# Kernel tuning notes

Measured on AMD Instinct MI355X. Metric: run time of the kernel, lower is better.

## Reference

```python
import jax, jax.numpy as jnp
import numpy as np

TAU = 1.0      # temperature for gumbel-softmax
EPS = 1e-12    # F.normalize eps


def _l2norm(v, axis):
    n = jnp.sqrt(jnp.sum(v * v, axis=axis, keepdims=True))
    return v / jnp.maximum(n, EPS)


def setup_inputs() -> dict:
    key = jax.random.key(0)
    k1, k2, k3, k4 = jax.random.split(key, 4)
    b, c, h, w, n = 8, 512, 64, 64, 1024
    x = jax.random.normal(k1, (b, c, h, w), dtype=jnp.float32)
    centers = jax.random.normal(k2, (n, c), dtype=jnp.float32)          # VQ codebook
    clusters = jax.random.normal(k3, (n, c), dtype=jnp.float32)         # ClusterLookup param
    gumbel_noise = jax.random.gumbel(k4, (b, n, h, w), dtype=jnp.float32)
    return {"x": x, "centers": centers, "clusters": clusters, "gumbel_noise": gumbel_noise}


def reference(x, centers, clusters, gumbel_noise):
    # similarity logits: [b, n, h, w]
    inner = jnp.einsum('bchw,nc->bnhw', x, centers)
    # hard gumbel-softmax (straight-through) over code dim
    y_soft = jax.nn.softmax((inner + gumbel_noise) / TAU, axis=1)
    idx = jnp.argmax(y_soft, axis=1)                                     # [b, h, w]
    y_hard = jax.nn.one_hot(idx, centers.shape[0], axis=1, dtype=y_soft.dtype)
    one_hot = y_hard - jax.lax.stop_gradient(y_soft) + y_soft            # [b, n, h, w]
    # quantized features: codebook lookup expressed as einsum
    z_q = jnp.einsum('bnhw,nd->bdhw', one_hot, centers)                  # [b, c, h, w]
    # ClusterLookup(z_q, alpha=None, is_direct=False)
    nf = _l2norm(z_q, axis=1)
    ncl = _l2norm(clusters, axis=1)
    ip = jnp.einsum('bchw,nc->bnhw', nf, ncl)                            # cluster logits
    preds = jnp.argmax(ip, axis=1)                                       # [b, h, w] int
    probs = jax.nn.one_hot(preds, clusters.shape[0], axis=1, dtype=ip.dtype)
    cluster_loss = -jnp.mean(jnp.sum(probs * ip, axis=1))
    return (cluster_loss, preds, ip, z_q)
```

## Files before the change

kernel.cpp:

```cpp
#include <hip/hip_runtime.h>
#include <math.h>

#define C 512
#define HW 4096
#define N 1024
#define NPIX 32768
#define MARGIN 2.0f
#define BLKPX 64
#define WAVES 4

typedef short s16x8 __attribute__((ext_vector_type(8)));
typedef float f32x4 __attribute__((ext_vector_type(4)));

__device__ inline unsigned short f2bf(float f) {
    unsigned int u = __float_as_uint(f);
    return (unsigned short)((u + 0x7FFFu + ((u >> 16) & 1u)) >> 16);
}
__device__ inline float h2f(unsigned short u) {
    _Float16 h; __builtin_memcpy(&h, &u, 2); return (float)h;
}
__device__ inline unsigned short f2h(float f) {
    _Float16 h = (_Float16)f; unsigned short u; __builtin_memcpy(&u, &h, 2); return u;
}
__device__ inline unsigned int mono(float v) {
    unsigned int u = __float_as_uint(v);
    return (u & 0x80000000u) ? ~u : (u | 0x80000000u);
}
__device__ inline int xsw(int p, int G) {
    return p * 512 + ((G ^ (((p >> 2) & 7) ^ ((p & 3) << 1))) << 2);
}

__global__ __launch_bounds__(64) void k_norms(const float* __restrict__ centers,
                                              const float* __restrict__ clusters,
                                              float* __restrict__ cnorm,
                                              float* __restrict__ clnorm) {
    int r = blockIdx.x;
    const float* src = (r < N) ? (centers + (size_t)r * C) : (clusters + (size_t)(r - N) * C);
    int lane = threadIdx.x;
    float s = 0.f;
    for (int k = lane; k < C; k += 64) { float v = src[k]; s += v * v; }
    #pragma unroll
    for (int m = 1; m < 64; m <<= 1) s += __shfl_xor(s, m, 64);
    if (lane == 0) {
        float nrm = sqrtf(s);
        if (nrm < 1e-12f) nrm = 1e-12f;
        if (r < N) cnorm[r] = nrm; else clnorm[r - N] = nrm;
    }
}

__global__ __launch_bounds__(256) void k_gemmM(const float* __restrict__ centers,
                                               const float* __restrict__ clusters,
                                               const float* __restrict__ cnorm,
                                               const float* __restrict__ clnorm,
                                               float* __restrict__ M) {
    __shared__ float as[32][68];
    __shared__ float bs[32][68];
    int tid = threadIdx.x;
    int tx = tid & 15, ty = tid >> 4;
    int i0 = blockIdx.x * 64, j0 = blockIdx.y * 64;
    int lrow = tid >> 2, lkq = (tid & 3) * 8;
    float acc[4][4] = {};
    for (int kc = 0; kc < C; kc += 32) {
        float4 a0 = *(const float4*)(centers + (size_t)(i0 + lrow) * C + kc + lkq);
        float4 a1 = *(const float4*)(centers + (size_t)(i0 + lrow) * C + kc + lkq + 4);
        float4 b0 = *(const float4*)(clusters + (size_t)(j0 + lrow) * C + kc + lkq);
        float4 b1 = *(const float4*)(clusters + (size_t)(j0 + lrow) * C + kc + lkq + 4);
        __syncthreads();
        as[lkq+0][lrow]=a0.x; as[lkq+1][lrow]=a0.y; as[lkq+2][lrow]=a0.z; as[lkq+3][lrow]=a0.w;
        as[lkq+4][lrow]=a1.x; as[lkq+5][lrow]=a1.y; as[lkq+6][lrow]=a1.z; as[lkq+7][lrow]=a1.w;
        bs[lkq+0][lrow]=b0.x; bs[lkq+1][lrow]=b0.y; bs[lkq+2][lrow]=b0.z; bs[lkq+3][lrow]=b0.w;
        bs[lkq+4][lrow]=b1.x; bs[lkq+5][lrow]=b1.y; bs[lkq+6][lrow]=b1.z; bs[lkq+7][lrow]=b1.w;
        __syncthreads();
        #pragma unroll
        for (int k = 0; k < 32; k += 4) {
            float av[4][4], bv[4][4];
            #pragma unroll
            for (int kk = 0; kk < 4; ++kk) {
                float4 ta = *(const float4*)&as[k+kk][tx*4];
                float4 tb = *(const float4*)&bs[k+kk][ty*4];
                av[kk][0]=ta.x; av[kk][1]=ta.y; av[kk][2]=ta.z; av[kk][3]=ta.w;
                bv[kk][0]=tb.x; bv[kk][1]=tb.y; bv[kk][2]=tb.z; bv[kk][3]=tb.w;
            }
            #pragma unroll
            for (int kk = 0; kk < 4; ++kk)
                #pragma unroll
                for (int ii = 0; ii < 4; ++ii)
                    #pragma unroll
                    for (int jj = 0; jj < 4; ++jj)
                        acc[ii][jj] = fmaf(av[kk][ii], bv[kk][jj], acc[ii][jj]);
        }
    }
    float rci[4], rcj[4];
    #pragma unroll
    for (int ii = 0; ii < 4; ++ii) rci[ii] = cnorm[i0 + tx*4 + ii];
    #pragma unroll
    for (int jj = 0; jj < 4; ++jj) rcj[jj] = clnorm[j0 + ty*4 + jj];
    #pragma unroll
    for (int ii = 0; ii < 4; ++ii)
        #pragma unroll
        for (int jj = 0; jj < 4; ++jj)
            M[(size_t)(i0 + tx*4 + ii) * N + (j0 + ty*4 + jj)] = acc[ii][jj] / (rci[ii] * rcj[jj]);
}

__global__ __launch_bounds__(256) void k_rowstat(const float* __restrict__ M,
                                                 float* __restrict__ rowmax,
                                                 int* __restrict__ rowarg) {
    __shared__ float sv[256];
    __shared__ int   sa[256];
    int i = blockIdx.x, tid = threadIdx.x;
    float bv = -INFINITY; int ba = 0;
    for (int j = tid; j < N; j += 256) {
        float v = M[(size_t)i * N + j];
        if (v > bv || (v == bv && j < ba)) { bv = v; ba = j; }
    }
    sv[tid] = bv; sa[tid] = ba;
    __syncthreads();
    for (int s = 128; s > 0; s >>= 1) {
        if (tid < s) {
            float v = sv[tid + s]; int a = sa[tid + s];
            if (v > sv[tid] || (v == sv[tid] && a < sa[tid])) { sv[tid] = v; sa[tid] = a; }
        }
        __syncthreads();
    }
    if (tid == 0) { rowmax[i] = sv[0]; rowarg[i] = sa[0]; }
}

__global__ __launch_bounds__(64) void k_cenfrag(const float* __restrict__ centers,
                                                unsigned short* __restrict__ cenB) {
    int f = blockIdx.x;
    int nt = f >> 4, kt = f & 15;
    int lane = threadIdx.x;
    int r = lane & 15, g = lane >> 4;
    const float* src = centers + (size_t)(nt * 16 + r) * C + kt * 32 + g * 4;
    float4 lo = *(const float4*)src;
    float4 hi = *(const float4*)(src + 16);
    union { unsigned short us[8]; uint4 q; } u;
    u.us[0]=f2bf(lo.x); u.us[1]=f2bf(lo.y); u.us[2]=f2bf(lo.z); u.us[3]=f2bf(lo.w);
    u.us[4]=f2bf(hi.x); u.us[5]=f2bf(hi.y); u.us[6]=f2bf(hi.z); u.us[7]=f2bf(hi.w);
    *(uint4*)(cenB + ((size_t)f * 64 + lane) * 8) = u.q;
}

__global__ __launch_bounds__(256, 1) void k_fused(const float* __restrict__ x,
                                                  const unsigned short* __restrict__ cenB,
                                                  const float* __restrict__ gumbel,
                                                  const float* __restrict__ centers,
                                                  int* __restrict__ idxb) {
    __shared__ float xs[BLKPX * 512];
    __shared__ unsigned short cen[16 * 512];
    __shared__ unsigned long long pixkey[BLKPX];
    __shared__ unsigned int candlist[WAVES][256];
    __shared__ int candcount[WAVES];

    int tid = threadIdx.x;
    int lane = tid & 63, w = tid >> 6;
    int r = lane & 15, g = lane >> 4;

    int p0 = blockIdx.x * BLKPX;
    int b = p0 >> 12, hw0 = p0 & (HW - 1);

    if (tid < BLKPX) pixkey[tid] = 0ull;
    if (tid < WAVES) candcount[tid] = 0;

    const uint4* cb = (const uint4*)cenB;
    uint4* cl = (uint4*)cen;
    #pragma unroll
    for (int j = 0; j < 4; ++j) cl[j * 256 + tid] = cb[j * 256 + tid];

    const float* xb = x + (size_t)b * C * HW + hw0;
    {
        int q = tid & 15, k0 = tid >> 4;
        #pragma unroll
        for (int kk = 0; kk < 32; ++kk) {
            int k = kk * 16 + k0;
            float4 v = *(const float4*)(xb + (size_t)k * HW + q * 4);
            int G = k >> 2, e = k & 3;
            xs[xsw(q * 4 + 0, G) + e] = v.x;
            xs[xsw(q * 4 + 1, G) + e] = v.y;
            xs[xsw(q * 4 + 2, G) + e] = v.z;
            xs[xsw(q * 4 + 3, G) + e] = v.w;
        }
    }
    __syncthreads();

    uint4 cr0 = cb[1024 + tid], cr1 = cb[1280 + tid], cr2 = cb[1536 + tid], cr3 = cb[1792 + tid];
    const float* gbase = gumbel + (size_t)b * N * HW + hw0 + w * 16 + g * 4;
    float4 gv_c = *(const float4*)(gbase + (size_t)r * HW);
    float4 gv_n = *(const float4*)(gbase + (size_t)(16 + r) * HW);

    s16x8 a[16];
    #pragma unroll
    for (int kt = 0; kt < 16; ++kt) {
        float4 lo = *(const float4*)&xs[xsw(w * 16 + r, kt * 8 + g)];
        float4 hi = *(const float4*)&xs[xsw(w * 16 + r, kt * 8 + 4 + g)];
        s16x8 t;
        t[0] = (short)f2bf(lo.x); t[1] = (short)f2bf(lo.y);
        t[2] = (short)f2bf(lo.z); t[3] = (short)f2bf(lo.w);
        t[4] = (short)f2bf(hi.x); t[5] = (short)f2bf(hi.y);
        t[6] = (short)f2bf(hi.z); t[7] = (short)f2bf(hi.w);
        a[kt] = t;
    }

    float m4[4] = {-INFINITY, -INFINITY, -INFINITY, -INFINITY};
    for (int ntc = 0; ntc < 8; ++ntc) {
        unsigned int keepH[16];
        #pragma unroll
        for (int s = 0; s < 8; ++s) {
            int nt = ntc * 8 + s;
            int ntf = (nt + 2 <= 63) ? nt + 2 : 63;
            float4 gv_f = *(const float4*)(gbase + (size_t)(ntf * 16 + r) * HW);
            const s16x8* bp = (const s16x8*)cen + lane;
            f32x4 acc0 = {0.f, 0.f, 0.f, 0.f};
            f32x4 acc1 = {0.f, 0.f, 0.f, 0.f};
            #pragma unroll
            for (int kt = 0; kt < 16; kt += 2) {
                s16x8 b0 = bp[kt * 64];
                s16x8 b1 = bp[(kt + 1) * 64];
                acc0 = __builtin_amdgcn_mfma_f32_16x16x32_bf16(a[kt],     b0, acc0, 0, 0, 0);
                acc1 = __builtin_amdgcn_mfma_f32_16x16x32_bf16(a[kt + 1], b1, acc1, 0, 0, 0);
            }
            float v0 = acc0[0] + acc1[0] + gv_c.x;
            float v1 = acc0[1] + acc1[1] + gv_c.y;
            float v2 = acc0[2] + acc1[2] + gv_c.z;
            float v3 = acc0[3] + acc1[3] + gv_c.w;
            m4[0] = fmaxf(m4[0], v0); m4[1] = fmaxf(m4[1], v1);
            m4[2] = fmaxf(m4[2], v2); m4[3] = fmaxf(m4[3], v3);
            keepH[s * 2]     = (unsigned int)f2h(v0) | ((unsigned int)f2h(v1) << 16);
            keepH[s * 2 + 1] = (unsigned int)f2h(v2) | ((unsigned int)f2h(v3) << 16);
            __builtin_amdgcn_s_barrier();
            __builtin_amdgcn_sched_barrier(0);
            cl[tid] = cr0; cl[256 + tid] = cr1; cl[512 + tid] = cr2; cl[768 + tid] = cr3;
            {
                const uint4* src = cb + (size_t)ntf * 1024;
                cr0 = src[tid]; cr1 = src[256 + tid]; cr2 = src[512 + tid]; cr3 = src[768 + tid];
            }
            asm volatile("s_waitcnt lgkmcnt(0)" ::: "memory");
            __builtin_amdgcn_s_barrier();
            __builtin_amdgcn_sched_barrier(0);
            gv_c = gv_n; gv_n = gv_f;
        }
        #pragma unroll
        for (int s2 = 1; s2 < 16; s2 <<= 1) {
            #pragma unroll
            for (int j = 0; j < 4; ++j) m4[j] = fmaxf(m4[j], __shfl_xor(m4[j], s2, 64));
        }
        float thr[4];
        #pragma unroll
        for (int j = 0; j < 4; ++j) thr[j] = m4[j] - MARGIN;
        #pragma unroll
        for (int s = 0; s < 8; ++s) {
            int nn = (ntc * 8 + s) * 16 + r;
            #pragma unroll
            for (int j2 = 0; j2 < 2; ++j2) {
                unsigned int pk = keepH[s * 2 + j2];
                float lo = h2f((unsigned short)(pk & 0xFFFFu));
                float hi = h2f((unsigned short)(pk >> 16));
                if (lo >= thr[j2 * 2]) {
                    int pos = atomicAdd(&candcount[w], 1);
                    if (pos < 256) candlist[w][pos] =
                        (unsigned int)nn | ((unsigned int)(w * 16 + g * 4 + j2 * 2) << 10);
                }
                if (hi >= thr[j2 * 2 + 1]) {
                    int pos = atomicAdd(&candcount[w], 1);
                    if (pos < 256) candlist[w][pos] =
                        (unsigned int)nn | ((unsigned int)(w * 16 + g * 4 + j2 * 2 + 1) << 10);
                }
            }
        }
    }

    int cc = candcount[w]; if (cc > 256) cc = 256;
    int sl = lane & 15, cg = lane >> 4;
    for (int t0 = 0; t0 < cc; t0 += 4) {
        int c = t0 + cg;
        bool valid = c < cc;
        unsigned int e = candlist[w][valid ? c : 0];
        int n = (int)(e & 1023u), pl = (int)(e >> 10);
        const float* cenr = centers + (size_t)n * C;
        float s = 0.f;
        #pragma unroll
        for (int m = 0; m < 8; ++m) {
            int G = sl + (m << 4);
            float4 xv = *(const float4*)&xs[xsw(pl, G)];
            float4 cv = *(const float4*)(cenr + (G << 2));
            s = fmaf(xv.x, cv.x, s); s = fmaf(xv.y, cv.y, s);
            s = fmaf(xv.z, cv.z, s); s = fmaf(xv.w, cv.w, s);
        }
        #pragma unroll
        for (int s2 = 1; s2 < 16; s2 <<= 1) s += __shfl_xor(s, s2, 64);
        if (valid && sl == 0) {
            float val = s + gumbel[((size_t)b * N + n) * HW + hw0 + pl];
            unsigned long long key = ((unsigned long long)mono(val) << 32) | (unsigned int)(1023 - n);
            atomicMax(&pixkey[pl], key);
        }
    }
    __syncthreads();
    if (tid < BLKPX) idxb[p0 + tid] = 1023 - (int)(unsigned int)(pixkey[tid] & 0xFFFFFFFFull);
}

__global__ __launch_bounds__(256) void k_preds(const int* __restrict__ idxb,
                                               const float* __restrict__ rowmax,
                                               const int* __restrict__ rowarg,
                                               float* __restrict__ preds_out,
                                               float* __restrict__ partial) {
    __shared__ float sv[256];
    int gid = blockIdx.x * 256 + threadIdx.x;
    int i = idxb[gid];
    preds_out[gid] = (float)rowarg[i];
    sv[threadIdx.x] = rowmax[i];
    __syncthreads();
    for (int s = 128; s > 0; s >>= 1) {
        if (threadIdx.x < s) sv[threadIdx.x] += sv[threadIdx.x + s];
        __syncthreads();
    }
    if (threadIdx.x == 0) partial[blockIdx.x] = sv[0];
}

__global__ __launch_bounds__(256) void k_gather(const float* __restrict__ src, int ncols,
                                                const int* __restrict__ idx,
                                                float* __restrict__ dst) {
    __shared__ float rows[64][65];
    int tile = blockIdx.x;
    int col0 = blockIdx.y * 64;
    int tid = threadIdx.x;
    int lane = tid & 63, w = tid >> 6;
    int b = tile >> 6, hw0 = (tile & 63) << 6;
    #pragma unroll
    for (int r8 = 0; r8 < 16; ++r8) {
        int r = w * 16 + r8;
        int row = idx[tile * 64 + r];
        rows[r][lane] = src[(size_t)row * ncols + col0 + lane];
    }
    __syncthreads();
    #pragma unroll
    for (int jj = 0; jj < 16; ++jj) {
        int j = col0 + w * 16 + jj;
        dst[((size_t)b * ncols + j) * HW + hw0 + lane] = rows[lane][w * 16 + jj];
    }
}

__global__ __launch_bounds__(128) void k_loss(const float* __restrict__ partial,
                                              float* __restrict__ out) {
    __shared__ float sv[128];
    sv[threadIdx.x] = partial[threadIdx.x];
    __syncthreads();
    for (int s = 64; s > 0; s >>= 1) {
        if (threadIdx.x < s) sv[threadIdx.x] += sv[threadIdx.x + s];
        __syncthreads();
    }
    if (threadIdx.x == 0) out[0] = -(sv[0] / 32768.0f);
}

extern "C" void kernel_launch(void* const* d_in, const int* in_sizes, int n_in,
                              void* d_out, int out_size, void* d_ws, size_t ws_size,
                              hipStream_t stream) {
    const float* x        = (const float*)d_in[0];
    const float* centers  = (const float*)d_in[1];
    const float* clusters = (const float*)d_in[2];
    const float* gumbel   = (const float*)d_in[3];
    float* out = (float*)d_out;

    char* w = (char*)d_ws;
    int*   idxb    = (int*)w;
    float* cnorm   = (float*)(w + 131072);
    float* clnorm  = cnorm + 1024;
    float* rowmax  = clnorm + 1024;
    int*   rowarg  = (int*)(rowmax + 1024);
    float* partial = (float*)(rowarg + 1024);
    float* M       = (float*)(w + 262144);
    unsigned short* cenB = (unsigned short*)(w + 4456448);

    float* out_loss  = out;
    float* out_preds = out + 1;
    float* out_ip    = out + 1 + 32768;
    float* out_zq    = out + 1 + 32768 + (size_t)N * NPIX;

    k_norms  <<<2048, 64, 0, stream>>>(centers, clusters, cnorm, clnorm);
    k_gemmM  <<<dim3(16, 16), 256, 0, stream>>>(centers, clusters, cnorm, clnorm, M);
    k_rowstat<<<1024, 256, 0, stream>>>(M, rowmax, rowarg);
    k_cenfrag<<<1024, 64, 0, stream>>>(centers, cenB);
    k_fused  <<<512, 256, 0, stream>>>(x, cenB, gumbel, centers, idxb);
    k_preds  <<<128, 256, 0, stream>>>(idxb, rowmax, rowarg, out_preds, partial);
    k_gather <<<dim3(512, 16), 256, 0, stream>>>(M, N, idxb, out_ip);
    k_gather <<<dim3(512, 8),  256, 0, stream>>>(centers, C, idxb, out_zq);
    k_loss   <<<1, 128, 0, stream>>>(partial, out_loss);
}
```

Baseline: 247.3 us.

## Pre-transpose x into pixel-major scratch and split codebook across wave groups

Adds a transpose kernel that writes x as pixel-major [pixel][channel] into the z_q output buffer, used as scratch. The fused argmax kernel then loads A fragments straight from global memory and drops the 128KB x tile from shared memory. It now runs 512 threads per block, with two wave groups each scanning half of the codebook, and double-buffers codebook fragments with one barrier per step. The aim is much higher occupancy and less LDS pressure, at the cost of an extra full pass over x to build the transpose and more syncthreads.

```diff
diff --git a/kernel.cpp b/kernel.cpp
--- a/kernel.cpp
+++ b/kernel.cpp
@@ -6,8 +6,6 @@
 #define N 1024
 #define NPIX 32768
 #define MARGIN 2.0f
-#define BLKPX 64
-#define WAVES 4
 
 typedef short s16x8 __attribute__((ext_vector_type(8)));
 typedef float f32x4 __attribute__((ext_vector_type(4)));
@@ -25,9 +23,6 @@
 __device__ inline unsigned int mono(float v) {
     unsigned int u = __float_as_uint(v);
     return (u & 0x80000000u) ? ~u : (u | 0x80000000u);
-}
-__device__ inline int xsw(int p, int G) {
-    return p * 512 + ((G ^ (((p >> 2) & 7) ^ ((p & 3) << 1))) << 2);
 }
 
 __global__ __launch_bounds__(64) void k_norms(const float* __restrict__ centers,
@@ -125,6 +120,29 @@
     if (tid == 0) { rowmax[i] = sv[0]; rowarg[i] = sa[0]; }
 }
 
+__global__ __launch_bounds__(256) void k_prepT(const float* __restrict__ x,
+                                               float* __restrict__ xT) {
+    __shared__ float t[64][65];
+    int bidx = blockIdx.x;
+    int pt = bidx & 63, kt = (bidx >> 6) & 7, b = bidx >> 9;
+    int r = threadIdx.x >> 4, c4 = (threadIdx.x & 15) * 4;
+    const float* src = x + ((size_t)b * C + kt * 64) * HW + pt * 64;
+    #pragma unroll
+    for (int rr = 0; rr < 4; ++rr) {
+        int row = rr * 16 + r;
+        float4 v = *(const float4*)(src + (size_t)row * HW + c4);
+        t[row][c4] = v.x; t[row][c4+1] = v.y; t[row][c4+2] = v.z; t[row][c4+3] = v.w;
+    }
+    __syncthreads();
+    float* dst = xT + ((size_t)b * HW + pt * 64) * C + kt * 64;
+    #pragma unroll
+    for (int rr = 0; rr < 4; ++rr) {
+        int row = rr * 16 + r;
+        float4 v = { t[c4][row], t[c4+1][row], t[c4+2][row], t[c4+3][row] };
+        *(float4*)(dst + (size_t)row * C + c4) = v;
+    }
+}
+
 __global__ __launch_bounds__(64) void k_cenfrag(const float* __restrict__ centers,
                                                 unsigned short* __restrict__ cenB) {
     int f = blockIdx.x;
@@ -140,103 +158,85 @@
     *(uint4*)(cenB + ((size_t)f * 64 + lane) * 8) = u.q;
 }
 
-__global__ __launch_bounds__(256, 1) void k_fused(const float* __restrict__ x,
+__global__ __launch_bounds__(512, 4) void k_fused(const float* __restrict__ xT,
                                                   const unsigned short* __restrict__ cenB,
                                                   const float* __restrict__ gumbel,
                                                   const float* __restrict__ centers,
                                                   int* __restrict__ idxb) {
-    __shared__ float xs[BLKPX * 512];
-    __shared__ unsigned short cen[16 * 512];
-    __shared__ unsigned long long pixkey[BLKPX];
-    __shared__ unsigned int candlist[WAVES][256];
-    __shared__ int candcount[WAVES];
+    __shared__ uint4 cen4[2][2][1024];
+    __shared__ unsigned long long pixkey[64];
+    __shared__ unsigned int candlist[8][256];
+    __shared__ int candcount[8];
 
     int tid = threadIdx.x;
     int lane = tid & 63, w = tid >> 6;
     int r = lane & 15, g = lane >> 4;
-
-    int p0 = blockIdx.x * BLKPX;
+    int pt = w & 3, gr = w >> 2;
+
+    int p0 = blockIdx.x * 64;
     int b = p0 >> 12, hw0 = p0 & (HW - 1);
 
-    if (tid < BLKPX) pixkey[tid] = 0ull;
-    if (tid < WAVES) candcount[tid] = 0;
+    if (tid < 64) pixkey[tid] = 0ull;
+    if (tid < 8) candcount[tid] = 0;
+
+    s16x8 a[16];
+    {
+        const float* xrow = xT + (size_t)(p0 + pt * 16 + r) * C;
+        #pragma unroll
+        for (int kt = 0; kt < 16; ++kt) {
+            float4 lo = *(const float4*)(xrow + kt * 32 + g * 4);
+            float4 hi = *(const float4*)(xrow + kt * 32 + 16 + g * 4);
+            s16x8 t;
+            t[0]=(short)f2bf(lo.x); t[1]=(short)f2bf(lo.y); t[2]=(short)f2bf(lo.z); t[3]=(short)f2bf(lo.w);
+            t[4]=(short)f2bf(hi.x); t[5]=(short)f2bf(hi.y); t[6]=(short)f2bf(hi.z); t[7]=(short)f2bf(hi.w);
+            a[kt] = t;
+        }
+    }
 
     const uint4* cb = (const uint4*)cenB;
-    uint4* cl = (uint4*)cen;
-    #pragma unroll
-    for (int j = 0; j < 4; ++j) cl[j * 256 + tid] = cb[j * 256 + tid];
-
-    const float* xb = x + (size_t)b * C * HW + hw0;
     {
-        int q = tid & 15, k0 = tid >> 4;
-        #pragma unroll
-        for (int kk = 0; kk < 32; ++kk) {
-            int k = kk * 16 + k0;
-            float4 v = *(const float4*)(xb + (size_t)k * HW + q * 4);
-            int G = k >> 2, e = k & 3;
-            xs[xsw(q * 4 + 0, G) + e] = v.x;
-            xs[xsw(q * 4 + 1, G) + e] = v.y;
-            xs[xsw(q * 4 + 2, G) + e] = v.z;
-            xs[xsw(q * 4 + 3, G) + e] = v.w;
-        }
-    }
-    __syncthreads();
-
-    uint4 cr0 = cb[1024 + tid], cr1 = cb[1280 + tid], cr2 = cb[1536 + tid], cr3 = cb[1792 + tid];
-    const float* gbase = gumbel + (size_t)b * N * HW + hw0 + w * 16 + g * 4;
-    float4 gv_c = *(const float4*)(gbase + (size_t)r * HW);
-    float4 gv_n = *(const float4*)(gbase + (size_t)(16 + r) * HW);
-
-    s16x8 a[16];
-    #pragma unroll
-    for (int kt = 0; kt < 16; ++kt) {
-        float4 lo = *(const float4*)&xs[xsw(w * 16 + r, kt * 8 + g)];
-        float4 hi = *(const float4*)&xs[xsw(w * 16 + r, kt * 8 + 4 + g)];
-        s16x8 t;
-        t[0] = (short)f2bf(lo.x); t[1] = (short)f2bf(lo.y);
-        t[2] = (short)f2bf(lo.z); t[3] = (short)f2bf(lo.w);
-        t[4] = (short)f2bf(hi.x); t[5] = (short)f2bf(hi.y);
-        t[6] = (short)f2bf(hi.z); t[7] = (short)f2bf(hi.w);
-        a[kt] = t;
-    }
+        const uint4* src = cb + (size_t)(gr * 32) * 1024 + pt * 256 + lane;
+        uint4* dst = &cen4[gr][0][pt * 256 + lane];
+        #pragma unroll
+        for (int i = 0; i < 4; ++i) dst[i * 64] = src[i * 64];
+    }
+    __syncthreads();
 
     float m4[4] = {-INFINITY, -INFINITY, -INFINITY, -INFINITY};
-    for (int ntc = 0; ntc < 8; ++ntc) {
-        unsigned int keepH[16];
-        #pragma unroll
-        for (int s = 0; s < 8; ++s) {
-            int nt = ntc * 8 + s;
-            int ntf = (nt + 2 <= 63) ? nt + 2 : 63;
-            float4 gv_f = *(const float4*)(gbase + (size_t)(ntf * 16 + r) * HW);
-            const s16x8* bp = (const s16x8*)cen + lane;
-            f32x4 acc0 = {0.f, 0.f, 0.f, 0.f};
-            f32x4 acc1 = {0.f, 0.f, 0.f, 0.f};
+    int cur = 0;
+    const float* gpx = gumbel + (size_t)b * N * HW + hw0 + pt * 16 + g * 4;
+
+    for (int tc = 0; tc < 8; ++tc) {
+        unsigned int keepH[8];
+        #pragma unroll
+        for (int s = 0; s < 4; ++s) {
+            int t = tc * 4 + s;
+            int tn = t + 1;
+            uint4 cr0, cr1, cr2, cr3;
+            if (tn < 32) {
+                const uint4* src = cb + (size_t)(gr * 32 + tn) * 1024 + pt * 256 + lane;
+                cr0 = src[0]; cr1 = src[64]; cr2 = src[128]; cr3 = src[192];
+            }
+            float4 gv = *(const float4*)(gpx + (size_t)((gr * 32 + t) * 16 + r) * HW);
+            const s16x8* bp = (const s16x8*)&cen4[gr][cur][0] + lane;
+            f32x4 acc0 = {0.f,0.f,0.f,0.f}, acc1 = {0.f,0.f,0.f,0.f};
             #pragma unroll
             for (int kt = 0; kt < 16; kt += 2) {
-                s16x8 b0 = bp[kt * 64];
-                s16x8 b1 = bp[(kt + 1) * 64];
-                acc0 = __builtin_amdgcn_mfma_f32_16x16x32_bf16(a[kt],     b0, acc0, 0, 0, 0);
-                acc1 = __builtin_amdgcn_mfma_f32_16x16x32_bf16(a[kt + 1], b1, acc1, 0, 0, 0);
-            }
-            float v0 = acc0[0] + acc1[0] + gv_c.x;
-            float v1 = acc0[1] + acc1[1] + gv_c.y;
-            float v2 = acc0[2] + acc1[2] + gv_c.z;
-            float v3 = acc0[3] + acc1[3] + gv_c.w;
-            m4[0] = fmaxf(m4[0], v0); m4[1] = fmaxf(m4[1], v1);
-            m4[2] = fmaxf(m4[2], v2); m4[3] = fmaxf(m4[3], v3);
-            keepH[s * 2]     = (unsigned int)f2h(v0) | ((unsigned int)f2h(v1) << 16);
-            keepH[s * 2 + 1] = (unsigned int)f2h(v2) | ((unsigned int)f2h(v3) << 16);
-            __builtin_amdgcn_s_barrier();
-            __builtin_amdgcn_sched_barrier(0);
-            cl[tid] = cr0; cl[256 + tid] = cr1; cl[512 + tid] = cr2; cl[768 + tid] = cr3;
-            {
-                const uint4* src = cb + (size_t)ntf * 1024;
-                cr0 = src[tid]; cr1 = src[256 + tid]; cr2 = src[512 + tid]; cr3 = src[768 + tid];
-            }
-            asm volatile("s_waitcnt lgkmcnt(0)" ::: "memory");
-            __builtin_amdgcn_s_barrier();
-            __builtin_amdgcn_sched_barrier(0);
-            gv_c = gv_n; gv_n = gv_f;
+                acc0 = __builtin_amdgcn_mfma_f32_16x16x32_bf16(a[kt],   bp[kt*64],     acc0, 0,0,0);
+                acc1 = __builtin_amdgcn_mfma_f32_16x16x32_bf16(a[kt+1], bp[(kt+1)*64], acc1, 0,0,0);
+            }
+            float v0 = acc0[0]+acc1[0]+gv.x, v1 = acc0[1]+acc1[1]+gv.y;
+            float v2 = acc0[2]+acc1[2]+gv.z, v3 = acc0[3]+acc1[3]+gv.w;
+            m4[0]=fmaxf(m4[0],v0); m4[1]=fmaxf(m4[1],v1);
+            m4[2]=fmaxf(m4[2],v2); m4[3]=fmaxf(m4[3],v3);
+            keepH[s*2]   = (unsigned int)f2h(v0) | ((unsigned int)f2h(v1) << 16);
+            keepH[s*2+1] = (unsigned int)f2h(v2) | ((unsigned int)f2h(v3) << 16);
+            if (tn < 32) {
+                uint4* dst = &cen4[gr][cur ^ 1][pt * 256 + lane];
+                dst[0] = cr0; dst[64] = cr1; dst[128] = cr2; dst[192] = cr3;
+            }
+            __syncthreads();
+            cur ^= 1;
         }
         #pragma unroll
         for (int s2 = 1; s2 < 16; s2 <<= 1) {
@@ -247,8 +247,8 @@
         #pragma unroll
         for (int j = 0; j < 4; ++j) thr[j] = m4[j] - MARGIN;
         #pragma unroll
-        for (int s = 0; s < 8; ++s) {
-            int nn = (ntc * 8 + s) * 16 + r;
+        for (int s = 0; s < 4; ++s) {
+            int nn = ((gr * 32 + tc * 4 + s) << 4) + r;
             #pragma unroll
             for (int j2 = 0; j2 < 2; ++j2) {
                 unsigned int pk = keepH[s * 2 + j2];
@@ -257,12 +257,12 @@
                 if (lo >= thr[j2 * 2]) {
                     int pos = atomicAdd(&candcount[w], 1);
                     if (pos < 256) candlist[w][pos] =
-                        (unsigned int)nn | ((unsigned int)(w * 16 + g * 4 + j2 * 2) << 10);
+                        (unsigned int)nn | ((unsigned int)(pt * 16 + g * 4 + j2 * 2) << 10);
                 }
                 if (hi >= thr[j2 * 2 + 1]) {
                     int pos = atomicAdd(&candcount[w], 1);
                     if (pos < 256) candlist[w][pos] =
-                        (unsigned int)nn | ((unsigned int)(w * 16 + g * 4 + j2 * 2 + 1) << 10);
+                        (unsigned int)nn | ((unsigned int)(pt * 16 + g * 4 + j2 * 2 + 1) << 10);
                 }
             }
         }
@@ -275,12 +275,13 @@
         bool valid = c < cc;
         unsigned int e = candlist[w][valid ? c : 0];
         int n = (int)(e & 1023u), pl = (int)(e >> 10);
+        const float* xr = xT + (size_t)(p0 + pl) * C;
         const float* cenr = centers + (size_t)n * C;
         float s = 0.f;
         #pragma unroll
         for (int m = 0; m < 8; ++m) {
             int G = sl + (m << 4);
-            float4 xv = *(const float4*)&xs[xsw(pl, G)];
+            float4 xv = *(const float4*)(xr + (G << 2));
             float4 cv = *(const float4*)(cenr + (G << 2));
             s = fmaf(xv.x, cv.x, s); s = fmaf(xv.y, cv.y, s);
             s = fmaf(xv.z, cv.z, s); s = fmaf(xv.w, cv.w, s);
@@ -294,7 +295,7 @@
         }
     }
     __syncthreads();
-    if (tid < BLKPX) idxb[p0 + tid] = 1023 - (int)(unsigned int)(pixkey[tid] & 0xFFFFFFFFull);
+    if (tid < 64) idxb[p0 + tid] = 1023 - (int)(unsigned int)(pixkey[tid] & 0xFFFFFFFFull);
 }
 
 __global__ __launch_bounds__(256) void k_preds(const int* __restrict__ idxb,
@@ -374,11 +375,14 @@
     float* out_ip    = out + 1 + 32768;
     float* out_zq    = out + 1 + 32768 + (size_t)N * NPIX;
 
+    float* xT = out_zq;
+
     k_norms  <<<2048, 64, 0, stream>>>(centers, clusters, cnorm, clnorm);
     k_gemmM  <<<dim3(16, 16), 256, 0, stream>>>(centers, clusters, cnorm, clnorm, M);
     k_rowstat<<<1024, 256, 0, stream>>>(M, rowmax, rowarg);
     k_cenfrag<<<1024, 64, 0, stream>>>(centers, cenB);
-    k_fused  <<<512, 256, 0, stream>>>(x, cenB, gumbel, centers, idxb);
+    k_prepT  <<<4096, 256, 0, stream>>>(x, xT);
+    k_fused  <<<512, 512, 0, stream>>>(xT, cenB, gumbel, centers, idxb);
     k_preds  <<<128, 256, 0, stream>>>(idxb, rowmax, rowarg, out_preds, partial);
     k_gather <<<dim3(512, 16), 256, 0, stream>>>(M, N, idxb, out_ip);
     k_gather <<<dim3(512, 8),  256, 0, stream>>>(centers, C, idxb, out_zq);
```

New measurement: 295.8 us. 1.2x slower.
